# Performance work log

Measured on AMD Instinct MI355X. Metric: run time of the kernel, lower is better.

Reference implementation:

```python
import jax, jax.numpy as jnp
import numpy as np

NEG_INF = -1e9


def _mask_dim1(a, lengths):
    # a: [B, L, X]; mask positions i >= lengths[b] along dim 1
    idx = jnp.arange(a.shape[1])[None, :, None]
    return jnp.where(idx < lengths[:, None, None], a, NEG_INF)


def setup_inputs() -> dict:
    key = jax.random.key(0)
    k1, k2, k3, k4 = jax.random.split(key, 4)
    B, Lq, Ld, H = 32, 1024, 1024, 1024
    q = jax.random.normal(k1, (B, Lq, H), dtype=jnp.float32)
    d = jax.random.normal(k2, (B, Ld, H), dtype=jnp.float32)
    q_len = jax.random.randint(k3, (B,), 1, Lq + 1)
    d_len = jax.random.randint(k4, (B,), 1, Ld + 1)
    return {"q": q, "d": d, "q_len": q_len, "d_len": d_len}


def reference(q, d, q_len, d_len):
    # a: [B, Lq, Ld] affinity matrix
    a = jnp.einsum("bqh,bdh->bqd", q, d)
    # softmax over query positions (dim 1), masked by q_len
    aq = jax.nn.softmax(_mask_dim1(a, q_len), axis=1)                 # [B, Lq, Ld]
    # softmax over document positions (dim 1 of a^T), masked by d_len
    ad = jax.nn.softmax(_mask_dim1(a.transpose(0, 2, 1), d_len), axis=1)  # [B, Ld, Lq]
    sd = jnp.einsum("bqh,bqd->bhd", q, aq)   # [B, H, Ld]
    sq = jnp.einsum("bdh,bdq->bhq", d, ad)   # [B, H, Lq]
    cd = jnp.einsum("bhq,bqd->bhd", sq, aq)  # [B, H, Ld]
    return (cd.transpose(0, 2, 1), sq.transpose(0, 2, 1), sd.transpose(0, 2, 1))
```

## Files before the change

### kernel.cpp

```cpp
#include <hip/hip_runtime.h>


constexpr int BATCH = 32;
constexpr int L  = 1024;
constexpr int HD = 1024;

constexpr int BM = 64, BN = 64, BK = 16;

__global__ __launch_bounds__(256) void affinity_kernel(
    const float* __restrict__ q, const float* __restrict__ d,
    float* __restrict__ A) {
  __shared__ float As[BK][BM + 1];
  __shared__ float Bs[BK][BN + 1];
  const int b  = blockIdx.z;
  const int m0 = blockIdx.y * BM;
  const int n0 = blockIdx.x * BN;
  const int tid = threadIdx.x;
  const int tx = tid % 16, ty = tid / 16;
  const float* qb = q + (size_t)b * L * HD;
  const float* db = d + (size_t)b * L * HD;
  float acc[4][4] = {};
  const int lrow = tid / 4;
  const int lk   = (tid % 4) * 4;
  for (int k0 = 0; k0 < HD; k0 += BK) {
    const float4 av = *(const float4*)(qb + (size_t)(m0 + lrow) * HD + k0 + lk);
    const float4 bv = *(const float4*)(db + (size_t)(n0 + lrow) * HD + k0 + lk);
    As[lk + 0][lrow] = av.x; As[lk + 1][lrow] = av.y;
    As[lk + 2][lrow] = av.z; As[lk + 3][lrow] = av.w;
    Bs[lk + 0][lrow] = bv.x; Bs[lk + 1][lrow] = bv.y;
    Bs[lk + 2][lrow] = bv.z; Bs[lk + 3][lrow] = bv.w;
    __syncthreads();
#pragma unroll
    for (int k = 0; k < BK; ++k) {
      float a[4], bb[4];
#pragma unroll
      for (int i = 0; i < 4; ++i) a[i] = As[k][ty * 4 + i];
#pragma unroll
      for (int j = 0; j < 4; ++j) bb[j] = Bs[k][tx * 4 + j];
#pragma unroll
      for (int i = 0; i < 4; ++i)
#pragma unroll
        for (int j = 0; j < 4; ++j) acc[i][j] += a[i] * bb[j];
    }
    __syncthreads();
  }
  float* Ab = A + (size_t)b * L * L;
#pragma unroll
  for (int i = 0; i < 4; ++i) {
    const int row = m0 + ty * 4 + i;
#pragma unroll
    for (int j = 0; j < 4; ++j)
      Ab[(size_t)row * L + n0 + tx * 4 + j] = acc[i][j];
  }
}

__global__ __launch_bounds__(256) void row_stats_kernel(
    const float* __restrict__ A, const int* __restrict__ d_len,
    float* __restrict__ m_out, float* __restrict__ s_out) {
  const int wave = threadIdx.x / 64, lane = threadIdx.x % 64;
  const int row = blockIdx.x * 4 + wave;
  const int b = row / L;
  const int len = d_len[b];
  const float* base = A + (size_t)row * L;
  float m = -1e30f;
  for (int k = lane; k < len; k += 64) m = fmaxf(m, base[k]);
#pragma unroll
  for (int off = 32; off > 0; off >>= 1) m = fmaxf(m, __shfl_xor(m, off, 64));
  float s = 0.f;
  for (int k = lane; k < len; k += 64) s += __expf(base[k] - m);
#pragma unroll
  for (int off = 32; off > 0; off >>= 1) s += __shfl_xor(s, off, 64);
  if (lane == 0) { m_out[row] = m; s_out[row] = s; }
}

__global__ __launch_bounds__(256) void col_stats_kernel(
    const float* __restrict__ A, const int* __restrict__ q_len,
    float* __restrict__ m_out, float* __restrict__ s_out) {
  const int col = blockIdx.x * 256 + threadIdx.x;
  const int b = col / L, di = col % L;
  const int len = q_len[b];
  const float* base = A + (size_t)b * L * L + di;
  float m = -1e30f, s = 0.f;
  for (int k = 0; k < len; ++k) {
    const float v = base[(size_t)k * L];
    const float mn = fmaxf(m, v);
    s = s * __expf(m - mn) + __expf(v - mn);
    m = mn;
  }
  m_out[col] = m;
  s_out[col] = s;
}

template <bool TRANSA>
__global__ __launch_bounds__(256) void norm_gemm_kernel(
    const float* __restrict__ A, const float* __restrict__ m_arr,
    const float* __restrict__ s_arr, const int* __restrict__ len_arr,
    const float* __restrict__ Bmat, float* __restrict__ C) {
  __shared__ float Ps[BK][BM + 1];
  __shared__ float Bs[BK][BN + 1];
  const int b  = blockIdx.z;
  const int m0 = blockIdx.y * BM;
  const int n0 = blockIdx.x * BN;
  const int tid = threadIdx.x;
  const int tx = tid % 16, ty = tid / 16;
  const int len = len_arr[b];
  const float* Ab = A + (size_t)b * L * L;
  const float* Bb = Bmat + (size_t)b * L * HD;
  float acc[4][4] = {};
  for (int k0 = 0; k0 < L; k0 += BK) {
    if (TRANSA) {
      const int kb = tid / 64;
      const int r  = tid % 64;
      const float mm = m_arr[(size_t)b * L + m0 + r];
#pragma unroll
      for (int i = 0; i < 4; ++i) {
        const int kk = kb + i * 4;
        const int kg = k0 + kk;
        const float v = Ab[(size_t)kg * L + m0 + r];
        Ps[kk][r] = (kg < len) ? __expf(v - mm) : 0.f;
      }
    } else {
      const int r  = tid / 4;
      const int kk = (tid % 4) * 4;
      const float4 v = *(const float4*)(Ab + (size_t)(m0 + r) * L + k0 + kk);
      const float mm = m_arr[(size_t)b * L + m0 + r];
      Ps[kk + 0][r] = (k0 + kk + 0 < len) ? __expf(v.x - mm) : 0.f;
      Ps[kk + 1][r] = (k0 + kk + 1 < len) ? __expf(v.y - mm) : 0.f;
      Ps[kk + 2][r] = (k0 + kk + 2 < len) ? __expf(v.z - mm) : 0.f;
      Ps[kk + 3][r] = (k0 + kk + 3 < len) ? __expf(v.w - mm) : 0.f;
    }
#pragma unroll
    for (int i = 0; i < 4; ++i) {
      const int e = tid + i * 256;
      const int h = e % 64, k = e / 64;
      Bs[k][h] = Bb[(size_t)(k0 + k) * HD + n0 + h];
    }
    __syncthreads();
#pragma unroll
    for (int k = 0; k < BK; ++k) {
      float a[4], bb[4];
#pragma unroll
      for (int i = 0; i < 4; ++i) a[i] = Ps[k][ty * 4 + i];
#pragma unroll
      for (int j = 0; j < 4; ++j) bb[j] = Bs[k][tx * 4 + j];
#pragma unroll
      for (int i = 0; i < 4; ++i)
#pragma unroll
        for (int j = 0; j < 4; ++j) acc[i][j] += a[i] * bb[j];
    }
    __syncthreads();
  }
#pragma unroll
  for (int i = 0; i < 4; ++i) {
    const int row = m0 + ty * 4 + i;
    const float inv = 1.f / s_arr[(size_t)b * L + row];
#pragma unroll
    for (int j = 0; j < 4; ++j)
      C[(size_t)b * L * HD + (size_t)row * HD + n0 + tx * 4 + j] =
          acc[i][j] * inv;
  }
}

extern "C" void kernel_launch(void* const* d_in, const int* in_sizes, int n_in,
                              void* d_out, int out_size, void* d_ws, size_t ws_size,
                              hipStream_t stream) {
  const float* q     = (const float*)d_in[0];
  const float* d     = (const float*)d_in[1];
  const int*   q_len = (const int*)d_in[2];
  const int*   d_len = (const int*)d_in[3];
  float* out = (float*)d_out;

  float* A   = (float*)d_ws;
  const size_t aElems = (size_t)BATCH * L * L;
  float* m_d = A + aElems;
  float* s_d = m_d + (size_t)BATCH * L;
  float* m_q = s_d + (size_t)BATCH * L;
  float* s_q = m_q + (size_t)BATCH * L;

  dim3 gA(L / BN, L / BM, BATCH);
  affinity_kernel<<<gA, 256, 0, stream>>>(q, d, A);

  row_stats_kernel<<<dim3(BATCH * L / 4), 256, 0, stream>>>(A, d_len, m_d, s_d);
  col_stats_kernel<<<dim3(BATCH * L / 256), 256, 0, stream>>>(A, q_len, m_q, s_q);

  float* cdT = out;
  float* sqT = out + (size_t)BATCH * L * HD;
  float* sdT = sqT + (size_t)BATCH * L * HD;

  dim3 gN(HD / BN, L / BM, BATCH);
  norm_gemm_kernel<false><<<gN, 256, 0, stream>>>(A, m_d, s_d, d_len, d, sqT);
  norm_gemm_kernel<true><<<gN, 256, 0, stream>>>(A, m_q, s_q, q_len, q, sdT);
  norm_gemm_kernel<true><<<gN, 256, 0, stream>>>(A, m_q, s_q, q_len, sqT, cdT);
}
```

Before: 5.996 ms.

## Unify GEMMs into 128x128 register-tiled double-buffered kernel with swizzled LDS

Replaces the separate affinity and normalized GEMM kernels with one templated GEMM that uses 128x128 tiles and an 8x8 per-thread register block. Shared memory is double-buffered, with global loads for the next tile prefetched into registers while the current tile computes, and LDS columns are XOR-swizzled so float4 reads avoid bank conflicts. Global loads and stores are vectorized as float4. This raises arithmetic intensity and hides load latency, at the cost of more registers per thread and fewer blocks per batch.

```diff
diff --git a/kernel.cpp b/kernel.cpp
--- a/kernel.cpp
+++ b/kernel.cpp
@@ -5,52 +5,181 @@
 constexpr int L  = 1024;
 constexpr int HD = 1024;
 
-constexpr int BM = 64, BN = 64, BK = 16;
-
-__global__ __launch_bounds__(256) void affinity_kernel(
-    const float* __restrict__ q, const float* __restrict__ d,
-    float* __restrict__ A) {
-  __shared__ float As[BK][BM + 1];
-  __shared__ float Bs[BK][BN + 1];
+constexpr int BM = 128, BN = 128, BK = 16;
+constexpr int NT = L / BK;
+
+__device__ __forceinline__ int swzmask(int k) {
+  return ((k & 4) << 2) | (k & 8);
+}
+
+template <int MODE>
+__global__ __launch_bounds__(256) void gemm_kernel(
+    const float* __restrict__ Asrc, const float* __restrict__ Bsrc,
+    const float* __restrict__ m_arr, const float* __restrict__ s_arr,
+    const int* __restrict__ len_arr, float* __restrict__ C) {
+  __shared__ float As[2][BK][BM];
+  __shared__ float Bs[2][BK][BN];
+
   const int b  = blockIdx.z;
   const int m0 = blockIdx.y * BM;
   const int n0 = blockIdx.x * BN;
-  const int tid = threadIdx.x;
-  const int tx = tid % 16, ty = tid / 16;
-  const float* qb = q + (size_t)b * L * HD;
-  const float* db = d + (size_t)b * L * HD;
-  float acc[4][4] = {};
-  const int lrow = tid / 4;
-  const int lk   = (tid % 4) * 4;
-  for (int k0 = 0; k0 < HD; k0 += BK) {
-    const float4 av = *(const float4*)(qb + (size_t)(m0 + lrow) * HD + k0 + lk);
-    const float4 bv = *(const float4*)(db + (size_t)(n0 + lrow) * HD + k0 + lk);
-    As[lk + 0][lrow] = av.x; As[lk + 1][lrow] = av.y;
-    As[lk + 2][lrow] = av.z; As[lk + 3][lrow] = av.w;
-    Bs[lk + 0][lrow] = bv.x; Bs[lk + 1][lrow] = bv.y;
-    Bs[lk + 2][lrow] = bv.z; Bs[lk + 3][lrow] = bv.w;
+  const int tid = (int)threadIdx.x;
+  const int tx = tid & 15, ty = tid >> 4;
+
+  const int len = (MODE == 0) ? L : len_arr[b];
+
+  const int sr = tid >> 2;
+  const int sk = (tid & 3) << 2;
+  const int kd = tid >> 5;
+  const int c4 = (tid & 31) << 2;
+
+  const float* aR0 = nullptr; const float* aR1 = nullptr;
+  const float* aCol = nullptr;
+  float mA0 = 0.f, mA1 = 0.f;
+  float4 mCol = make_float4(0.f, 0.f, 0.f, 0.f);
+
+  if (MODE == 0) {
+    aR0 = Asrc + (size_t)b * L * HD + (size_t)(m0 + sr) * HD;
+    aR1 = aR0 + (size_t)64 * HD;
+  } else if (MODE == 1) {
+    aR0 = Asrc + (size_t)b * L * L + (size_t)(m0 + sr) * L;
+    aR1 = aR0 + (size_t)64 * L;
+    mA0 = m_arr[b * L + m0 + sr];
+    mA1 = m_arr[b * L + m0 + sr + 64];
+  } else {
+    aCol = Asrc + (size_t)b * L * L + m0 + c4;
+    mCol = *(const float4*)(m_arr + b * L + m0 + c4);
+  }
+
+  const float* bR0 = nullptr; const float* bR1 = nullptr;
+  const float* bCol = nullptr;
+  if (MODE == 0) {
+    bR0 = Bsrc + (size_t)b * L * HD + (size_t)(n0 + sr) * HD;
+    bR1 = bR0 + (size_t)64 * HD;
+  } else {
+    bCol = Bsrc + (size_t)b * L * HD + n0 + c4;
+  }
+
+  float4 va0, va1, vb0, vb1;
+
+  auto loadTiles = [&](int k0) {
+    if (MODE == 2) {
+      va0 = *(const float4*)(aCol + (size_t)(k0 + kd) * L);
+      va1 = *(const float4*)(aCol + (size_t)(k0 + kd + 8) * L);
+    } else {
+      va0 = *(const float4*)(aR0 + k0 + sk);
+      va1 = *(const float4*)(aR1 + k0 + sk);
+    }
+    if (MODE == 0) {
+      vb0 = *(const float4*)(bR0 + k0 + sk);
+      vb1 = *(const float4*)(bR1 + k0 + sk);
+    } else {
+      vb0 = *(const float4*)(bCol + (size_t)(k0 + kd) * HD);
+      vb1 = *(const float4*)(bCol + (size_t)(k0 + kd + 8) * HD);
+    }
+  };
+
+  auto writeTiles = [&](int buf, int k0) {
+    float (*as)[BM] = As[buf];
+    float (*bs)[BN] = Bs[buf];
+    if (MODE == 2) {
+#pragma unroll
+      for (int j = 0; j < 2; ++j) {
+        const int k = kd + j * 8;
+        const float4 v = j ? va1 : va0;
+        const bool ok = (k0 + k) < len;
+        float4 e;
+        e.x = ok ? __expf(v.x - mCol.x) : 0.f;
+        e.y = ok ? __expf(v.y - mCol.y) : 0.f;
+        e.z = ok ? __expf(v.z - mCol.z) : 0.f;
+        e.w = ok ? __expf(v.w - mCol.w) : 0.f;
+        *(float4*)&as[k][c4 ^ swzmask(k)] = e;
+      }
+    } else if (MODE == 1) {
+#pragma unroll
+      for (int i = 0; i < 4; ++i) {
+        const int k = sk + i;
+        const bool ok = (k0 + k) < len;
+        const int c = sr ^ swzmask(k);
+        as[k][c]      = ok ? __expf(((const float*)&va0)[i] - mA0) : 0.f;
+        as[k][c + 64] = ok ? __expf(((const float*)&va1)[i] - mA1) : 0.f;
+      }
+    } else {
+#pragma unroll
+      for (int i = 0; i < 4; ++i) {
+        const int k = sk + i;
+        const int c = sr ^ swzmask(k);
+        as[k][c]      = ((const float*)&va0)[i];
+        as[k][c + 64] = ((const float*)&va1)[i];
+      }
+    }
+    if (MODE == 0) {
+#pragma unroll
+      for (int i = 0; i < 4; ++i) {
+        const int k = sk + i;
+        const int c = sr ^ swzmask(k);
+        bs[k][c]      = ((const float*)&vb0)[i];
+        bs[k][c + 64] = ((const float*)&vb1)[i];
+      }
+    } else {
+#pragma unroll
+      for (int j = 0; j < 2; ++j) {
+        const int k = kd + j * 8;
+        const float4 v = j ? vb1 : vb0;
+        *(float4*)&bs[k][c4 ^ swzmask(k)] = v;
+      }
+    }
+  };
+
+  float acc[8][8] = {};
+
+  loadTiles(0);
+  writeTiles(0, 0);
+  __syncthreads();
+
+  int cur = 0;
+  for (int t = 0; t < NT; ++t) {
+    const bool more = (t + 1 < NT);
+    if (more) loadTiles((t + 1) * BK);
+
+    const float (*as)[BM] = As[cur];
+    const float (*bs)[BN] = Bs[cur];
+#pragma unroll
+    for (int k = 0; k < BK; ++k) {
+      const int msk = swzmask(k);
+      const int ca = (ty << 2) ^ msk;
+      const int cb = (tx << 2) ^ msk;
+      const float4 a0 = *(const float4*)&as[k][ca];
+      const float4 a1 = *(const float4*)&as[k][ca + 64];
+      const float4 b0 = *(const float4*)&bs[k][cb];
+      const float4 b1 = *(const float4*)&bs[k][cb + 64];
+      const float a[8]  = {a0.x, a0.y, a0.z, a0.w, a1.x, a1.y, a1.z, a1.w};
+      const float bb[8] = {b0.x, b0.y, b0.z, b0.w, b1.x, b1.y, b1.z, b1.w};
+#pragma unroll
+      for (int i = 0; i < 8; ++i)
+#pragma unroll
+        for (int j = 0; j < 8; ++j) acc[i][j] += a[i] * bb[j];
+    }
+    if (more) writeTiles(cur ^ 1, (t + 1) * BK);
     __syncthreads();
-#pragma unroll
-    for (int k = 0; k < BK; ++k) {
-      float a[4], bb[4];
-#pragma unroll
-      for (int i = 0; i < 4; ++i) a[i] = As[k][ty * 4 + i];
-#pragma unroll
-      for (int j = 0; j < 4; ++j) bb[j] = Bs[k][tx * 4 + j];
-#pragma unroll
-      for (int i = 0; i < 4; ++i)
-#pragma unroll
-        for (int j = 0; j < 4; ++j) acc[i][j] += a[i] * bb[j];
-    }
-    __syncthreads();
-  }
-  float* Ab = A + (size_t)b * L * L;
-#pragma unroll
-  for (int i = 0; i < 4; ++i) {
-    const int row = m0 + ty * 4 + i;
-#pragma unroll
-    for (int j = 0; j < 4; ++j)
-      Ab[(size_t)row * L + n0 + tx * 4 + j] = acc[i][j];
+    cur ^= 1;
+  }
+
+  float* Cb = C + (size_t)b * L * HD;
+#pragma unroll
+  for (int ih = 0; ih < 2; ++ih) {
+#pragma unroll
+    for (int i = 0; i < 4; ++i) {
+      const int row = m0 + ih * 64 + (ty << 2) + i;
+      float sc = 1.f;
+      if (MODE != 0) sc = 1.f / s_arr[b * L + row];
+      const float* ar = acc[ih * 4 + i];
+      const float4 v0 = make_float4(ar[0] * sc, ar[1] * sc, ar[2] * sc, ar[3] * sc);
+      const float4 v1 = make_float4(ar[4] * sc, ar[5] * sc, ar[6] * sc, ar[7] * sc);
+      float* cp = Cb + (size_t)row * HD + n0 + (tx << 2);
+      *(float4*)cp = v0;
+      *(float4*)(cp + 64) = v1;
+    }
   }
 }
 
@@ -91,76 +220,6 @@
   s_out[col] = s;
 }
 
-template <bool TRANSA>
-__global__ __launch_bounds__(256) void norm_gemm_kernel(
-    const float* __restrict__ A, const float* __restrict__ m_arr,
-    const float* __restrict__ s_arr, const int* __restrict__ len_arr,
-    const float* __restrict__ Bmat, float* __restrict__ C) {
-  __shared__ float Ps[BK][BM + 1];
-  __shared__ float Bs[BK][BN + 1];
-  const int b  = blockIdx.z;
-  const int m0 = blockIdx.y * BM;
-  const int n0 = blockIdx.x * BN;
-  const int tid = threadIdx.x;
-  const int tx = tid % 16, ty = tid / 16;
-  const int len = len_arr[b];
-  const float* Ab = A + (size_t)b * L * L;
-  const float* Bb = Bmat + (size_t)b * L * HD;
-  float acc[4][4] = {};
-  for (int k0 = 0; k0 < L; k0 += BK) {
-    if (TRANSA) {
-      const int kb = tid / 64;
-      const int r  = tid % 64;
-      const float mm = m_arr[(size_t)b * L + m0 + r];
-#pragma unroll
-      for (int i = 0; i < 4; ++i) {
-        const int kk = kb + i * 4;
-        const int kg = k0 + kk;
-        const float v = Ab[(size_t)kg * L + m0 + r];
-        Ps[kk][r] = (kg < len) ? __expf(v - mm) : 0.f;
-      }
-    } else {
-      const int r  = tid / 4;
-      const int kk = (tid % 4) * 4;
-      const float4 v = *(const float4*)(Ab + (size_t)(m0 + r) * L + k0 + kk);
-      const float mm = m_arr[(size_t)b * L + m0 + r];
-      Ps[kk + 0][r] = (k0 + kk + 0 < len) ? __expf(v.x - mm) : 0.f;
-      Ps[kk + 1][r] = (k0 + kk + 1 < len) ? __expf(v.y - mm) : 0.f;
-      Ps[kk + 2][r] = (k0 + kk + 2 < len) ? __expf(v.z - mm) : 0.f;
-      Ps[kk + 3][r] = (k0 + kk + 3 < len) ? __expf(v.w - mm) : 0.f;
-    }
-#pragma unroll
-    for (int i = 0; i < 4; ++i) {
-      const int e = tid + i * 256;
-      const int h = e % 64, k = e / 64;
-      Bs[k][h] = Bb[(size_t)(k0 + k) * HD + n0 + h];
-    }
-    __syncthreads();
-#pragma unroll
-    for (int k = 0; k < BK; ++k) {
-      float a[4], bb[4];
-#pragma unroll
-      for (int i = 0; i < 4; ++i) a[i] = Ps[k][ty * 4 + i];
-#pragma unroll
-      for (int j = 0; j < 4; ++j) bb[j] = Bs[k][tx * 4 + j];
-#pragma unroll
-      for (int i = 0; i < 4; ++i)
-#pragma unroll
-        for (int j = 0; j < 4; ++j) acc[i][j] += a[i] * bb[j];
-    }
-    __syncthreads();
-  }
-#pragma unroll
-  for (int i = 0; i < 4; ++i) {
-    const int row = m0 + ty * 4 + i;
-    const float inv = 1.f / s_arr[(size_t)b * L + row];
-#pragma unroll
-    for (int j = 0; j < 4; ++j)
-      C[(size_t)b * L * HD + (size_t)row * HD + n0 + tx * 4 + j] =
-          acc[i][j] * inv;
-  }
-}
-
 extern "C" void kernel_launch(void* const* d_in, const int* in_sizes, int n_in,
                               void* d_out, int out_size, void* d_ws, size_t ws_size,
                               hipStream_t stream) {
@@ -178,7 +237,7 @@
   float* s_q = m_q + (size_t)BATCH * L;
 
   dim3 gA(L / BN, L / BM, BATCH);
-  affinity_kernel<<<gA, 256, 0, stream>>>(q, d, A);
+  gemm_kernel<0><<<gA, 256, 0, stream>>>(q, d, nullptr, nullptr, nullptr, A);
 
   row_stats_kernel<<<dim3(BATCH * L / 4), 256, 0, stream>>>(A, d_len, m_d, s_d);
   col_stats_kernel<<<dim3(BATCH * L / 256), 256, 0, stream>>>(A, q_len, m_q, s_q);
@@ -188,7 +247,7 @@
   float* sdT = sqT + (size_t)BATCH * L * HD;
 
   dim3 gN(HD / BN, L / BM, BATCH);
-  norm_gemm_kernel<false><<<gN, 256, 0, stream>>>(A, m_d, s_d, d_len, d, sqT);
-  norm_gemm_kernel<true><<<gN, 256, 0, stream>>>(A, m_q, s_q, q_len, q, sdT);
-  norm_gemm_kernel<true><<<gN, 256, 0, stream>>>(A, m_q, s_q, q_len, sqT, cdT);
-}
+  gemm_kernel<1><<<gN, 256, 0, stream>>>(A, d, m_d, s_d, d_len, sqT);
+  gemm_kernel<2><<<gN, 256, 0, stream>>>(A, q, m_q, s_q, q_len, sdT);
+  gemm_kernel<2><<<gN, 256, 0, stream>>>(A, sqT, m_q, s_q, q_len, cdT);
+}
```

New measurement: 5.250 ms. -12.4%, faster.
